# Performance work log

Measured on AMD Instinct MI355X. Metric: run time of the kernel, lower is better.

Reference implementation:

```python
import jax, jax.numpy as jnp
import numpy as np

E, H, BLOCK = 1024, 64, 2048

def setup_inputs() -> dict:
    key = jax.random.key(0)
    kx, kk, kq, kv = jax.random.split(key, 4)
    s = 1.0 / np.sqrt(E)
    return {
        "x": jax.random.normal(kx, (16, 2048, E), dtype=jnp.float32),
        "Wk": jax.random.uniform(kk, (E, H), jnp.float32, -s, s),
        "Wq": jax.random.uniform(kq, (E, H), jnp.float32, -s, s),
        "Wv": jax.random.uniform(kv, (E, H), jnp.float32, -s, s),
    }

def reference(x, Wk, Wq, Wv):
    B, T, C = x.shape
    k = x @ Wk  # [B,T,H]
    q = x @ Wq
    v = x @ Wv
    scale = jnp.asarray(H, x.dtype) ** -0.5
    wei = jnp.einsum("bth,bsh->bts", q, k) * scale  # [B,T,T]
    causal = jnp.tril(jnp.ones((T, T), dtype=bool))
    wei = jnp.where(causal, wei, -jnp.inf)
    wei = jax.nn.softmax(wei, axis=-1)
    # dropout is identity in eval mode
    return jnp.einsum("bts,bsh->bth", wei, v)
```

## Files before the change

kernel.cpp:

```cpp
#include <hip/hip_runtime.h>


typedef __bf16 bf16x8 __attribute__((ext_vector_type(8)));
typedef __bf16 bf16x4 __attribute__((ext_vector_type(4)));
typedef float f32x4 __attribute__((ext_vector_type(4)));

constexpr int kE = 1024;
constexpr int kH = 64;
constexpr int kT = 2048;
constexpr int kB = 16;
constexpr int kM = kB * kT;
constexpr float kQScale = 0.125f * 1.44269504088896340736f;

#define MFMA16(a, b, c) __builtin_amdgcn_mfma_f32_16x16x32_bf16((a), (b), (c), 0, 0, 0)

__global__ __launch_bounds__(256)
void prep_w(const float* __restrict__ Wq, const float* __restrict__ Wk,
            const float* __restrict__ Wv, __bf16* __restrict__ WbT)
{
    __shared__ float tl[64][65];
    const int mat = blockIdx.x >> 4;
    const int k0 = (blockIdx.x & 15) * 64;
    const float* src = (mat == 0) ? Wq : (mat == 1) ? Wk : Wv;

    const int t = threadIdx.x;
    const int kr = t >> 2;
    const int cg = (t & 3) * 16;
    #pragma unroll
    for (int i = 0; i < 4; ++i) {
        float4 v = *(const float4*)&src[(size_t)(k0 + kr) * kH + cg + 4 * i];
        tl[cg + 4 * i + 0][kr] = v.x;
        tl[cg + 4 * i + 1][kr] = v.y;
        tl[cg + 4 * i + 2][kr] = v.z;
        tl[cg + 4 * i + 3][kr] = v.w;
    }
    __syncthreads();
    const int nl = t >> 2;
    const int kg = (t & 3) * 16;
    bf16x8 o0, o1;
    #pragma unroll
    for (int j = 0; j < 8; ++j) {
        o0[j] = (__bf16)tl[nl][kg + j];
        o1[j] = (__bf16)tl[nl][kg + 8 + j];
    }
    *(bf16x8*)&WbT[(size_t)(mat * 64 + nl) * kE + k0 + kg] = o0;
    *(bf16x8*)&WbT[(size_t)(mat * 64 + nl) * kE + k0 + kg + 8] = o1;
}

__global__ __launch_bounds__(256)
void qkv(const float* __restrict__ x, const __bf16* __restrict__ WbT,
         __bf16* __restrict__ qo, __bf16* __restrict__ ko, __bf16* __restrict__ vT)
{
    __shared__ __align__(16) __bf16 As[64][72];
    __shared__ __align__(16) __bf16 Bs[192][72];

    const int t = threadIdx.x;
    const int lane = t & 63;
    const int w = t >> 6;
    const int l15 = lane & 15;
    const int q = lane >> 4;
    const int row0 = blockIdx.x * 64;

    f32x4 acc[4][3];
    #pragma unroll
    for (int mt = 0; mt < 4; ++mt)
        #pragma unroll
        for (int nt = 0; nt < 3; ++nt) acc[mt][nt] = (f32x4){0.f, 0.f, 0.f, 0.f};

    const int sm = t >> 2;
    const int sc = (t & 3) * 16;

    for (int k0 = 0; k0 < kE; k0 += 64) {
        {
            float4 v0 = *(const float4*)&x[(size_t)(row0 + sm) * kE + k0 + sc];
            float4 v1 = *(const float4*)&x[(size_t)(row0 + sm) * kE + k0 + sc + 4];
            float4 v2 = *(const float4*)&x[(size_t)(row0 + sm) * kE + k0 + sc + 8];
            float4 v3 = *(const float4*)&x[(size_t)(row0 + sm) * kE + k0 + sc + 12];
            bf16x8 b0, b1;
            b0[0] = (__bf16)v0.x; b0[1] = (__bf16)v0.y; b0[2] = (__bf16)v0.z; b0[3] = (__bf16)v0.w;
            b0[4] = (__bf16)v1.x; b0[5] = (__bf16)v1.y; b0[6] = (__bf16)v1.z; b0[7] = (__bf16)v1.w;
            b1[0] = (__bf16)v2.x; b1[1] = (__bf16)v2.y; b1[2] = (__bf16)v2.z; b1[3] = (__bf16)v2.w;
            b1[4] = (__bf16)v3.x; b1[5] = (__bf16)v3.y; b1[6] = (__bf16)v3.z; b1[7] = (__bf16)v3.w;
            *(bf16x8*)&As[sm][sc] = b0;
            *(bf16x8*)&As[sm][sc + 8] = b1;
        }
        #pragma unroll
        for (int j = 0; j < 6; ++j) {
            int id = t + 256 * j;
            int n = id >> 3;
            int kc = (id & 7) * 8;
            *(bf16x8*)&Bs[n][kc] = *(const bf16x8*)&WbT[(size_t)n * kE + k0 + kc];
        }
        __syncthreads();

        #pragma unroll
        for (int ks = 0; ks < 2; ++ks) {
            bf16x8 a4[4];
            #pragma unroll
            for (int mt = 0; mt < 4; ++mt)
                a4[mt] = *(const bf16x8*)&As[mt * 16 + l15][ks * 32 + q * 8];
            #pragma unroll
            for (int nt = 0; nt < 3; ++nt) {
                bf16x8 b = *(const bf16x8*)&Bs[w * 48 + nt * 16 + l15][ks * 32 + q * 8];
                #pragma unroll
                for (int mt = 0; mt < 4; ++mt)
                    acc[mt][nt] = MFMA16(a4[mt], b, acc[mt][nt]);
            }
        }
        __syncthreads();
    }

    const int batch = row0 >> 11;
    const int tr0 = row0 & 2047;
    #pragma unroll
    for (int nt = 0; nt < 3; ++nt) {
        const int col0 = w * 48 + nt * 16;
        const int mat = col0 >> 6;
        const int c = (col0 & 63) + l15;
        if (mat == 2) {
            #pragma unroll
            for (int mt = 0; mt < 4; ++mt) {
                const int trow = tr0 + mt * 16 + q * 4;
                bf16x4 pk;
                #pragma unroll
                for (int r = 0; r < 4; ++r) pk[r] = (__bf16)acc[mt][nt][r];
                *(bf16x4*)&vT[((size_t)batch * kH + c) * kT + trow] = pk;
            }
        } else {
            __bf16* dst = (mat == 0) ? qo : ko;
            const float sc_ = (mat == 0) ? kQScale : 1.0f;
            #pragma unroll
            for (int mt = 0; mt < 4; ++mt)
                #pragma unroll
                for (int r = 0; r < 4; ++r) {
                    const size_t row = row0 + mt * 16 + q * 4 + r;
                    dst[row * kH + c] = (__bf16)(acc[mt][nt][r] * sc_);
                }
        }
    }
}

__device__ __forceinline__ void load_kfrag(bf16x8 kf[8], const __bf16* kb,
                                           int s0, int l15, int Q)
{
    #pragma unroll
    for (int ks = 0; ks < 2; ++ks)
        #pragma unroll
        for (int nt = 0; nt < 4; ++nt)
            kf[ks * 4 + nt] =
                *(const bf16x8*)&kb[(size_t)(s0 + nt * 16 + l15) * kH + ks * 32 + Q * 8];
}

__global__ __launch_bounds__(64)
void attn(const __bf16* __restrict__ qm, const __bf16* __restrict__ km,
          const __bf16* __restrict__ vT, float* __restrict__ out)
{
    __shared__ __align__(16) __bf16 Ps[16][72];

    const int lane = threadIdx.x;
    const int l15 = lane & 15;
    const int Q = lane >> 4;

    const int batch = blockIdx.x & 15;
    const int q16 = 127 - (blockIdx.x >> 4);
    const int qrow = q16 * 16 + l15;
    const int last = q16 >> 2;

    const __bf16* qb = qm + (size_t)batch * kT * kH;
    const __bf16* kb = km + (size_t)batch * kT * kH;
    const __bf16* vb = vT + (size_t)batch * kH * kT;

    bf16x8 aq[2];
    aq[0] = *(const bf16x8*)&qb[(size_t)qrow * kH + Q * 8];
    aq[1] = *(const bf16x8*)&qb[(size_t)qrow * kH + 32 + Q * 8];

    f32x4 O[4];
    #pragma unroll
    for (int i = 0; i < 4; ++i) O[i] = (f32x4){0.f, 0.f, 0.f, 0.f};
    float m_ = -3.0e38f, l_ = 0.f;

    bf16x8 kfa[8], kfb[8];
    load_kfrag(kfa, kb, 0, l15, Q);

    auto step = [&](bf16x8 (&kcur)[8], bf16x8 (&knxt)[8], int kt) {
        const int s0 = kt * 64;
        bf16x8 vf[8];
        #pragma unroll
        for (int ht = 0; ht < 4; ++ht)
            #pragma unroll
            for (int ss = 0; ss < 2; ++ss)
                vf[ht * 2 + ss] =
                    *(const bf16x8*)&vb[(size_t)(ht * 16 + l15) * kT + s0 + ss * 32 + Q * 8];
        if (kt < last) load_kfrag(knxt, kb, s0 + 64, l15, Q);

        f32x4 sacc[4];
        #pragma unroll
        for (int nt = 0; nt < 4; ++nt) sacc[nt] = (f32x4){0.f, 0.f, 0.f, 0.f};
        #pragma unroll
        for (int ks = 0; ks < 2; ++ks)
            #pragma unroll
            for (int nt = 0; nt < 4; ++nt)
                sacc[nt] = MFMA16(kcur[ks * 4 + nt], aq[ks], sacc[nt]);

        if (kt == last) {
            #pragma unroll
            for (int nt = 0; nt < 4; ++nt)
                #pragma unroll
                for (int r = 0; r < 4; ++r)
                    if (s0 + nt * 16 + Q * 4 + r > qrow) sacc[nt][r] = -3.0e38f;
        }

        float mx = sacc[0][0];
        #pragma unroll
        for (int nt = 0; nt < 4; ++nt)
            #pragma unroll
            for (int r = 0; r < 4; ++r) mx = fmaxf(mx, sacc[nt][r]);
        mx = fmaxf(mx, __shfl_xor(mx, 16));
        mx = fmaxf(mx, __shfl_xor(mx, 32));
        const float mnew = fmaxf(m_, mx);
        const float alpha = __builtin_amdgcn_exp2f(m_ - mnew);
        float rs = 0.f;
        #pragma unroll
        for (int nt = 0; nt < 4; ++nt)
            #pragma unroll
            for (int r = 0; r < 4; ++r) {
                const float p = __builtin_amdgcn_exp2f(sacc[nt][r] - mnew);
                sacc[nt][r] = p;
                rs += p;
            }
        rs += __shfl_xor(rs, 16);
        rs += __shfl_xor(rs, 32);
        l_ = l_ * alpha + rs;
        m_ = mnew;
        #pragma unroll
        for (int ht = 0; ht < 4; ++ht) O[ht] *= alpha;

        #pragma unroll
        for (int nt = 0; nt < 4; ++nt) {
            bf16x4 pk;
            #pragma unroll
            for (int r = 0; r < 4; ++r) pk[r] = (__bf16)sacc[nt][r];
            *(bf16x4*)&Ps[l15][nt * 16 + Q * 4] = pk;
        }
        bf16x8 pb0 = *(const bf16x8*)&Ps[l15][Q * 8];
        bf16x8 pb1 = *(const bf16x8*)&Ps[l15][32 + Q * 8];

        #pragma unroll
        for (int ht = 0; ht < 4; ++ht) {
            O[ht] = MFMA16(vf[ht * 2 + 0], pb0, O[ht]);
            O[ht] = MFMA16(vf[ht * 2 + 1], pb1, O[ht]);
        }
    };

    for (int kt = 0; kt <= last; kt += 2) {
        step(kfa, kfb, kt);
        if (kt + 1 <= last) step(kfb, kfa, kt + 1);
    }

    const float inv = 1.0f / l_;
    float* orow = out + ((size_t)batch * kT + qrow) * kH;
    #pragma unroll
    for (int ht = 0; ht < 4; ++ht) {
        float4 o4;
        o4.x = O[ht][0] * inv; o4.y = O[ht][1] * inv;
        o4.z = O[ht][2] * inv; o4.w = O[ht][3] * inv;
        *(float4*)&orow[ht * 16 + Q * 4] = o4;
    }
}

extern "C" void kernel_launch(void* const* d_in, const int* in_sizes, int n_in,
                              void* d_out, int out_size, void* d_ws, size_t ws_size,
                              hipStream_t stream)
{
    (void)in_sizes; (void)n_in; (void)out_size; (void)ws_size;
    const float* x  = (const float*)d_in[0];
    const float* Wk = (const float*)d_in[1];
    const float* Wq = (const float*)d_in[2];
    const float* Wv = (const float*)d_in[3];

    __bf16* WbT = (__bf16*)d_ws;
    __bf16* qb  = WbT + (size_t)192 * kE;
    __bf16* kbuf = qb + (size_t)kM * kH;
    __bf16* vT   = kbuf + (size_t)kM * kH;

    prep_w<<<48, 256, 0, stream>>>(Wq, Wk, Wv, WbT);
    qkv<<<kM / 64, 256, 0, stream>>>(x, WbT, qb, kbuf, vT);
    attn<<<kB * 128, 64, 0, stream>>>(qb, kbuf, vT, (float*)d_out);
}
```

Before: 272.2 us.

## Share K/V tiles in LDS across four waves and drop LDS staging in QKV GEMM

The attention kernel now runs 256-thread blocks covering 64 query rows. Each 64-key K and V tile is loaded once into shared memory with register prefetch and shared by the four waves, where before each 16-row wave fetched K/V from global memory on its own. The QKV projection kernel drops its shared-memory staging and barriers and loads MFMA fragments directly from global memory with unroll 2. This trades global traffic for two barriers per key tile in attention and possibly less coalesced, redundant fragment loads in the GEMM. It also reduces the attention grid to 512 blocks, which coarsens load balancing across the causal triangle.

```diff
diff --git a/kernel.cpp b/kernel.cpp
--- a/kernel.cpp
+++ b/kernel.cpp
@@ -51,9 +51,6 @@
 void qkv(const float* __restrict__ x, const __bf16* __restrict__ WbT,
          __bf16* __restrict__ qo, __bf16* __restrict__ ko, __bf16* __restrict__ vT)
 {
-    __shared__ __align__(16) __bf16 As[64][72];
-    __shared__ __align__(16) __bf16 Bs[192][72];
-
     const int t = threadIdx.x;
     const int lane = t & 63;
     const int w = t >> 6;
@@ -67,47 +64,46 @@
         #pragma unroll
         for (int nt = 0; nt < 3; ++nt) acc[mt][nt] = (f32x4){0.f, 0.f, 0.f, 0.f};
 
-    const int sm = t >> 2;
-    const int sc = (t & 3) * 16;
-
+    const float* xrow[4];
+    #pragma unroll
+    for (int mt = 0; mt < 4; ++mt)
+        xrow[mt] = &x[(size_t)(row0 + mt * 16 + l15) * kE + q * 8];
+    const __bf16* brow[3];
+    #pragma unroll
+    for (int nt = 0; nt < 3; ++nt)
+        brow[nt] = &WbT[(size_t)(w * 48 + nt * 16 + l15) * kE + q * 8];
+
+    #pragma unroll 2
     for (int k0 = 0; k0 < kE; k0 += 64) {
-        {
-            float4 v0 = *(const float4*)&x[(size_t)(row0 + sm) * kE + k0 + sc];
-            float4 v1 = *(const float4*)&x[(size_t)(row0 + sm) * kE + k0 + sc + 4];
-            float4 v2 = *(const float4*)&x[(size_t)(row0 + sm) * kE + k0 + sc + 8];
-            float4 v3 = *(const float4*)&x[(size_t)(row0 + sm) * kE + k0 + sc + 12];
-            bf16x8 b0, b1;
-            b0[0] = (__bf16)v0.x; b0[1] = (__bf16)v0.y; b0[2] = (__bf16)v0.z; b0[3] = (__bf16)v0.w;
-            b0[4] = (__bf16)v1.x; b0[5] = (__bf16)v1.y; b0[6] = (__bf16)v1.z; b0[7] = (__bf16)v1.w;
-            b1[0] = (__bf16)v2.x; b1[1] = (__bf16)v2.y; b1[2] = (__bf16)v2.z; b1[3] = (__bf16)v2.w;
-            b1[4] = (__bf16)v3.x; b1[5] = (__bf16)v3.y; b1[6] = (__bf16)v3.z; b1[7] = (__bf16)v3.w;
-            *(bf16x8*)&As[sm][sc] = b0;
-            *(bf16x8*)&As[sm][sc + 8] = b1;
-        }
-        #pragma unroll
-        for (int j = 0; j < 6; ++j) {
-            int id = t + 256 * j;
-            int n = id >> 3;
-            int kc = (id & 7) * 8;
-            *(bf16x8*)&Bs[n][kc] = *(const bf16x8*)&WbT[(size_t)n * kE + k0 + kc];
-        }
-        __syncthreads();
-
-        #pragma unroll
-        for (int ks = 0; ks < 2; ++ks) {
-            bf16x8 a4[4];
-            #pragma unroll
-            for (int mt = 0; mt < 4; ++mt)
-                a4[mt] = *(const bf16x8*)&As[mt * 16 + l15][ks * 32 + q * 8];
-            #pragma unroll
-            for (int nt = 0; nt < 3; ++nt) {
-                bf16x8 b = *(const bf16x8*)&Bs[w * 48 + nt * 16 + l15][ks * 32 + q * 8];
+        bf16x8 bfrag[2][3];
+        #pragma unroll
+        for (int ks = 0; ks < 2; ++ks)
+            #pragma unroll
+            for (int nt = 0; nt < 3; ++nt)
+                bfrag[ks][nt] = *(const bf16x8*)&brow[nt][k0 + ks * 32];
+
+        bf16x8 afrag[2][4];
+        #pragma unroll
+        for (int mt = 0; mt < 4; ++mt)
+            #pragma unroll
+            for (int ks = 0; ks < 2; ++ks) {
+                float4 u0 = *(const float4*)&xrow[mt][k0 + ks * 32];
+                float4 u1 = *(const float4*)&xrow[mt][k0 + ks * 32 + 4];
+                bf16x8 a;
+                a[0] = (__bf16)u0.x; a[1] = (__bf16)u0.y;
+                a[2] = (__bf16)u0.z; a[3] = (__bf16)u0.w;
+                a[4] = (__bf16)u1.x; a[5] = (__bf16)u1.y;
+                a[6] = (__bf16)u1.z; a[7] = (__bf16)u1.w;
+                afrag[ks][mt] = a;
+            }
+
+        #pragma unroll
+        for (int ks = 0; ks < 2; ++ks)
+            #pragma unroll
+            for (int nt = 0; nt < 3; ++nt)
                 #pragma unroll
                 for (int mt = 0; mt < 4; ++mt)
-                    acc[mt][nt] = MFMA16(a4[mt], b, acc[mt][nt]);
-            }
-        }
-        __syncthreads();
+                    acc[mt][nt] = MFMA16(afrag[ks][mt], bfrag[ks][nt], acc[mt][nt]);
     }
 
     const int batch = row0 >> 11;
@@ -140,31 +136,24 @@
     }
 }
 
-__device__ __forceinline__ void load_kfrag(bf16x8 kf[8], const __bf16* kb,
-                                           int s0, int l15, int Q)
-{
-    #pragma unroll
-    for (int ks = 0; ks < 2; ++ks)
-        #pragma unroll
-        for (int nt = 0; nt < 4; ++nt)
-            kf[ks * 4 + nt] =
-                *(const bf16x8*)&kb[(size_t)(s0 + nt * 16 + l15) * kH + ks * 32 + Q * 8];
-}
-
-__global__ __launch_bounds__(64)
+__global__ __launch_bounds__(256)
 void attn(const __bf16* __restrict__ qm, const __bf16* __restrict__ km,
           const __bf16* __restrict__ vT, float* __restrict__ out)
 {
-    __shared__ __align__(16) __bf16 Ps[16][72];
-
-    const int lane = threadIdx.x;
+    __shared__ __align__(16) __bf16 Ks[64][72];
+    __shared__ __align__(16) __bf16 Vt[64][72];
+    __shared__ __align__(16) __bf16 Ps[4][16][72];
+
+    const int t = threadIdx.x;
+    const int lane = t & 63;
+    const int w = t >> 6;
     const int l15 = lane & 15;
     const int Q = lane >> 4;
 
     const int batch = blockIdx.x & 15;
-    const int q16 = 127 - (blockIdx.x >> 4);
-    const int qrow = q16 * 16 + l15;
-    const int last = q16 >> 2;
+    const int qi = 31 - (blockIdx.x >> 4);
+    const int q0 = qi * 64;
+    const int qrow = q0 + w * 16 + l15;
 
     const __bf16* qb = qm + (size_t)batch * kT * kH;
     const __bf16* kb = km + (size_t)batch * kT * kH;
@@ -179,19 +168,43 @@
     for (int i = 0; i < 4; ++i) O[i] = (f32x4){0.f, 0.f, 0.f, 0.f};
     float m_ = -3.0e38f, l_ = 0.f;
 
-    bf16x8 kfa[8], kfb[8];
-    load_kfrag(kfa, kb, 0, l15, Q);
-
-    auto step = [&](bf16x8 (&kcur)[8], bf16x8 (&knxt)[8], int kt) {
-        const int s0 = kt * 64;
-        bf16x8 vf[8];
+    const int sr = t >> 2;
+    const int scg = (t & 3) * 16;
+
+    bf16x8 k0r, k1r, v0r, v1r;
+    {
+        k0r = *(const bf16x8*)&kb[(size_t)sr * kH + scg];
+        k1r = *(const bf16x8*)&kb[(size_t)sr * kH + scg + 8];
+        v0r = *(const bf16x8*)&vb[(size_t)sr * kT + scg];
+        v1r = *(const bf16x8*)&vb[(size_t)sr * kT + scg + 8];
+    }
+
+    for (int kt = 0; kt <= qi; ++kt) {
+        *(bf16x8*)&Ks[sr][scg] = k0r;
+        *(bf16x8*)&Ks[sr][scg + 8] = k1r;
+        *(bf16x8*)&Vt[sr][scg] = v0r;
+        *(bf16x8*)&Vt[sr][scg + 8] = v1r;
+        __syncthreads();
+
+        if (kt < qi) {
+            const int sn = (kt + 1) * 64;
+            k0r = *(const bf16x8*)&kb[(size_t)(sn + sr) * kH + scg];
+            k1r = *(const bf16x8*)&kb[(size_t)(sn + sr) * kH + scg + 8];
+            v0r = *(const bf16x8*)&vb[(size_t)sr * kT + sn + scg];
+            v1r = *(const bf16x8*)&vb[(size_t)sr * kT + sn + scg + 8];
+        }
+
+        bf16x8 kf[8], vf[8];
+        #pragma unroll
+        for (int ks = 0; ks < 2; ++ks)
+            #pragma unroll
+            for (int nt = 0; nt < 4; ++nt)
+                kf[ks * 4 + nt] = *(const bf16x8*)&Ks[nt * 16 + l15][ks * 32 + Q * 8];
         #pragma unroll
         for (int ht = 0; ht < 4; ++ht)
             #pragma unroll
             for (int ss = 0; ss < 2; ++ss)
-                vf[ht * 2 + ss] =
-                    *(const bf16x8*)&vb[(size_t)(ht * 16 + l15) * kT + s0 + ss * 32 + Q * 8];
-        if (kt < last) load_kfrag(knxt, kb, s0 + 64, l15, Q);
+                vf[ht * 2 + ss] = *(const bf16x8*)&Vt[ht * 16 + l15][ss * 32 + Q * 8];
 
         f32x4 sacc[4];
         #pragma unroll
@@ -200,9 +213,10 @@
         for (int ks = 0; ks < 2; ++ks)
             #pragma unroll
             for (int nt = 0; nt < 4; ++nt)
-                sacc[nt] = MFMA16(kcur[ks * 4 + nt], aq[ks], sacc[nt]);
-
-        if (kt == last) {
+                sacc[nt] = MFMA16(kf[ks * 4 + nt], aq[ks], sacc[nt]);
+
+        if (kt == qi) {
+            const int s0 = kt * 64;
             #pragma unroll
             for (int nt = 0; nt < 4; ++nt)
                 #pragma unroll
@@ -240,21 +254,17 @@
             bf16x4 pk;
             #pragma unroll
             for (int r = 0; r < 4; ++r) pk[r] = (__bf16)sacc[nt][r];
-            *(bf16x4*)&Ps[l15][nt * 16 + Q * 4] = pk;
-        }
-        bf16x8 pb0 = *(const bf16x8*)&Ps[l15][Q * 8];
-        bf16x8 pb1 = *(const bf16x8*)&Ps[l15][32 + Q * 8];
+            *(bf16x4*)&Ps[w][l15][nt * 16 + Q * 4] = pk;
+        }
+        bf16x8 pb0 = *(const bf16x8*)&Ps[w][l15][Q * 8];
+        bf16x8 pb1 = *(const bf16x8*)&Ps[w][l15][32 + Q * 8];
 
         #pragma unroll
         for (int ht = 0; ht < 4; ++ht) {
             O[ht] = MFMA16(vf[ht * 2 + 0], pb0, O[ht]);
             O[ht] = MFMA16(vf[ht * 2 + 1], pb1, O[ht]);
         }
-    };
-
-    for (int kt = 0; kt <= last; kt += 2) {
-        step(kfa, kfb, kt);
-        if (kt + 1 <= last) step(kfb, kfa, kt + 1);
+        __syncthreads();
     }
 
     const float inv = 1.0f / l_;
@@ -278,12 +288,12 @@
     const float* Wq = (const float*)d_in[2];
     const float* Wv = (const float*)d_in[3];
 
-    __bf16* WbT = (__bf16*)d_ws;
-    __bf16* qb  = WbT + (size_t)192 * kE;
+    __bf16* WbT  = (__bf16*)d_ws;
+    __bf16* qb   = WbT + (size_t)192 * kE;
     __bf16* kbuf = qb + (size_t)kM * kH;
     __bf16* vT   = kbuf + (size_t)kM * kH;
 
     prep_w<<<48, 256, 0, stream>>>(Wq, Wk, Wv, WbT);
     qkv<<<kM / 64, 256, 0, stream>>>(x, WbT, qb, kbuf, vT);
-    attn<<<kB * 128, 64, 0, stream>>>(qb, kbuf, vT, (float*)d_out);
-}
+    attn<<<kB * 32, 256, 0, stream>>>(qb, kbuf, vT, (float*)d_out);
+}
```

Result: slower. 285.2 us (+4.8%).
